# Optimization experiments

Hardware: AMD Instinct MI355X
Metric: run time of the kernel (lower is better)

Reference implementation:

```python
import jax, jax.numpy as jnp
import numpy as np
from jax.scipy.special import logsumexp

SPARSITY = 0.0


def setup_inputs() -> dict:
    key = jax.random.key(0)
    k1, k2, k3, k4, k5 = jax.random.split(key, 5)
    N, M = 65536, 1024
    sample = jax.random.uniform(k1, (N, 2), dtype=jnp.float32)
    mu = jax.random.uniform(k2, (M, 2), dtype=jnp.float32)
    sigma_log = jax.random.uniform(k3, (M, 2), dtype=jnp.float32)
    theta = jax.random.normal(k4, (M,), dtype=jnp.float32)
    w = jax.random.normal(k5, (M, 1), dtype=jnp.float32)
    return {"sample": sample, "mu": mu, "sigma_log": sigma_log, "theta": theta, "w": w}


def reference(sample, mu, sigma_log, theta, w):
    # Anisotropic covariance entries: gamma_j = R(theta)^T diag(sig2) R(theta)
    sig2 = jnp.exp(-2.0 * sigma_log)            # [M,2], inverse variances
    a, b = sig2[:, 0], sig2[:, 1]
    c, s = jnp.cos(theta), jnp.sin(theta)
    g11 = a * c**2 + b * s**2                   # [M]
    g12 = (a - b) * c * s                       # [M]
    g22 = a * s**2 + b * c**2                   # [M]

    # Log weights: log_softmax(w) - sum(sigma_log) (normalization factor)
    wlog = jax.nn.log_softmax(w, axis=0)[:, 0] - sigma_log.sum(axis=1)  # [M]

    # All-pairs anisotropic quadratic form, fused per-coordinate (no [N,M,2] tensor)
    dx = sample[:, None, 0] - mu[None, :, 0]    # [N,M]
    dy = sample[:, None, 1] - mu[None, :, 1]    # [N,M]
    qf = g11 * dx * dx + 2.0 * g12 * dx * dy + g22 * dy * dy  # [N,M]

    # Log-density at each sample: logsumexp over mixture components
    ll = logsumexp(wlog[None, :] - qf, axis=1)  # [N]

    # Negative log-likelihood + sparsity penalty
    nll = -ll.sum() + SPARSITY * jnp.sqrt(jax.nn.softmax(w, axis=0)).sum()
    return nll
```

## Files before the change

### kernel.cpp

```cpp
#include <hip/hip_runtime.h>
#include <math.h>

#define LOG2E 1.4426950408889634f
#define LN2   0.6931471805599453f

typedef float v2f __attribute__((ext_vector_type(2)));

__global__ __launch_bounds__(1024) void gm_params(
    const float* __restrict__ mu,
    const float* __restrict__ sigma_log,
    const float* __restrict__ theta,
    const float* __restrict__ w,
    float* __restrict__ pp,
    float* __restrict__ out)
{
    const int j = threadIdx.x;
    const int lane = j & 63;
    const int wid  = j >> 6;

    const float wj = w[j];

    float e = __expf(wj);
    #pragma unroll
    for (int off = 32; off > 0; off >>= 1)
        e += __shfl_down(e, off, 64);

    __shared__ float ws[16];
    if (lane == 0) ws[wid] = e;
    __syncthreads();

    float tot = 0.0f;
    #pragma unroll
    for (int k = 0; k < 16; ++k) tot += ws[k];
    const float lse = __logf(tot);

    const float sl0 = sigma_log[2 * j + 0];
    const float sl1 = sigma_log[2 * j + 1];
    const float a = __expf(-2.0f * sl0);
    const float b = __expf(-2.0f * sl1);
    const float th = theta[j];
    const float c = __cosf(th);
    const float s = __sinf(th);

    const float g11 = a * c * c + b * s * s;
    const float g12 = (a - b) * c * s;
    const float g22 = a * s * s + b * c * c;

    const float mx = mu[2 * j + 0];
    const float my = mu[2 * j + 1];

    const float wlog = wj - lse - (sl0 + sl1);

    const float A = g11;
    const float B = 2.0f * g12;
    const float C = g22;
    const float D = -(2.0f * g11 * mx + 2.0f * g12 * my);
    const float E = -(2.0f * g12 * mx + 2.0f * g22 * my);
    const float F = g11 * mx * mx + 2.0f * g12 * mx * my + g22 * my * my;
    const float K = (wlog - F) * LOG2E;

    const int base = 12 * (j >> 1) + (j & 1);
    pp[base + 0]  = -A * LOG2E;
    pp[base + 2]  = -B * LOG2E;
    pp[base + 4]  = -C * LOG2E;
    pp[base + 6]  = -D * LOG2E;
    pp[base + 8]  = -E * LOG2E;
    pp[base + 10] = K;

    if (j == 0) out[0] = 0.0f;
}

__global__ __launch_bounds__(1024) void gm_main(
    const float* __restrict__ sample,
    const float* __restrict__ pp,
    float* __restrict__ out,
    int M)
{
    const int lane = threadIdx.x & 63;
    int chunk = __builtin_amdgcn_readfirstlane((int)(threadIdx.x >> 6));
    chunk &= 15;
    __builtin_assume(chunk >= 0 && chunk < 16);

    const int i = blockIdx.x * 64 + lane;

    const float2 sv = ((const float2*)sample)[i];
    const float sx = sv.x, sy = sv.y;
    const v2f xx2 = (v2f)(sx * sx);
    const v2f xy2 = (v2f)(sx * sy);
    const v2f yy2 = (v2f)(sy * sy);
    const v2f sx2 = (v2f)(sx);
    const v2f sy2 = (v2f)(sy);

    const int pairs = M >> 5;
    const v2f* __restrict__ rec = (const v2f*)(pp + 12 * (chunk * pairs));

    v2f acc[4];
    #pragma unroll
    for (int u = 0; u < 4; ++u) acc[u] = (v2f)(0.0f);

    for (int p = 0; p < pairs; p += 4) {
        #pragma unroll
        for (int u = 0; u < 4; ++u) {
            const v2f* r = rec + 6 * (p + u);
            v2f e = r[5];
            e = __builtin_elementwise_fma(r[0], xx2, e);
            e = __builtin_elementwise_fma(r[1], xy2, e);
            e = __builtin_elementwise_fma(r[2], yy2, e);
            e = __builtin_elementwise_fma(r[3], sx2, e);
            e = __builtin_elementwise_fma(r[4], sy2, e);
            v2f ex;
            ex.x = __builtin_amdgcn_exp2f(e.x);
            ex.y = __builtin_amdgcn_exp2f(e.y);
            acc[u] += ex;
        }
    }

    const v2f accv = (acc[0] + acc[1]) + (acc[2] + acc[3]);

    __shared__ float psum[16][64];
    psum[chunk][lane] = accv.x + accv.y;
    __syncthreads();

    if (threadIdx.x < 64) {
        const int s = threadIdx.x;
        float tot = 0.0f;
        #pragma unroll
        for (int k = 0; k < 16; ++k) tot += psum[k][s];
        float v = -LN2 * __builtin_amdgcn_logf(tot);
        #pragma unroll
        for (int off = 32; off > 0; off >>= 1)
            v += __shfl_down(v, off, 64);
        if (s == 0) atomicAdd(out, v);
    }
}

extern "C" void kernel_launch(void* const* d_in, const int* in_sizes, int n_in,
                              void* d_out, int out_size, void* d_ws, size_t ws_size,
                              hipStream_t stream) {
    const float* sample    = (const float*)d_in[0];
    const float* mu        = (const float*)d_in[1];
    const float* sigma_log = (const float*)d_in[2];
    const float* theta     = (const float*)d_in[3];
    const float* w         = (const float*)d_in[4];
    float* out = (float*)d_out;
    float* pp = (float*)d_ws;

    const int M = in_sizes[3];
    const int N = in_sizes[0] / 2;

    gm_params<<<1, M, 0, stream>>>(mu, sigma_log, theta, w, pp, out);

    const int grid = N / 64;
    gm_main<<<grid, 1024, 0, stream>>>(sample, pp, out, M);
}
```

Measured before the change: 81.58 us.

## Fuse parameter precompute into main kernel with per-block LDS records

Removes the separate single-block parameter kernel. Each of the 1024 main blocks now recomputes all M component coefficients (softmax, exp, sin/cos) and stores them in shared memory, then reads them as float4 from LDS instead of from global memory. The output is zeroed with a memset instead. This drops one kernel launch and the serial dependency between the two kernels, at the cost of redundant per-block transcendental work plus an extra block-wide sync.

```diff
diff --git a/kernel.cpp b/kernel.cpp
--- a/kernel.cpp
+++ b/kernel.cpp
@@ -6,84 +6,75 @@
 
 typedef float v2f __attribute__((ext_vector_type(2)));
 
-__global__ __launch_bounds__(1024) void gm_params(
+__global__ __launch_bounds__(1024) void gm_fused(
+    const float* __restrict__ sample,
     const float* __restrict__ mu,
     const float* __restrict__ sigma_log,
     const float* __restrict__ theta,
     const float* __restrict__ w,
-    float* __restrict__ pp,
-    float* __restrict__ out)
+    float* __restrict__ out,
+    int M)
 {
-    const int j = threadIdx.x;
-    const int lane = j & 63;
-    const int wid  = j >> 6;
+    __shared__ float4 recs4[512 * 3];
+    __shared__ float  ws[16];
+    __shared__ float  psum[16][64];
 
-    const float wj = w[j];
+    const int tid  = threadIdx.x;
+    const int lane = tid & 63;
+    const int wid  = tid >> 6;
 
+    const int i = blockIdx.x * 64 + lane;
+    const float2 sv = ((const float2*)sample)[i];
+
+    const float wj = w[tid];
     float e = __expf(wj);
     #pragma unroll
     for (int off = 32; off > 0; off >>= 1)
         e += __shfl_down(e, off, 64);
-
-    __shared__ float ws[16];
     if (lane == 0) ws[wid] = e;
     __syncthreads();
-
     float tot = 0.0f;
     #pragma unroll
     for (int k = 0; k < 16; ++k) tot += ws[k];
     const float lse = __logf(tot);
 
-    const float sl0 = sigma_log[2 * j + 0];
-    const float sl1 = sigma_log[2 * j + 1];
-    const float a = __expf(-2.0f * sl0);
-    const float b = __expf(-2.0f * sl1);
-    const float th = theta[j];
-    const float c = __cosf(th);
-    const float s = __sinf(th);
+    {
+        const float sl0 = sigma_log[2 * tid + 0];
+        const float sl1 = sigma_log[2 * tid + 1];
+        const float a = __expf(-2.0f * sl0);
+        const float b = __expf(-2.0f * sl1);
+        const float th = theta[tid];
+        const float c = __cosf(th);
+        const float s = __sinf(th);
 
-    const float g11 = a * c * c + b * s * s;
-    const float g12 = (a - b) * c * s;
-    const float g22 = a * s * s + b * c * c;
+        const float g11 = a * c * c + b * s * s;
+        const float g12 = (a - b) * c * s;
+        const float g22 = a * s * s + b * c * c;
 
-    const float mx = mu[2 * j + 0];
-    const float my = mu[2 * j + 1];
+        const float mx = mu[2 * tid + 0];
+        const float my = mu[2 * tid + 1];
 
-    const float wlog = wj - lse - (sl0 + sl1);
+        const float wlog = wj - lse - (sl0 + sl1);
 
-    const float A = g11;
-    const float B = 2.0f * g12;
-    const float C = g22;
-    const float D = -(2.0f * g11 * mx + 2.0f * g12 * my);
-    const float E = -(2.0f * g12 * mx + 2.0f * g22 * my);
-    const float F = g11 * mx * mx + 2.0f * g12 * mx * my + g22 * my * my;
-    const float K = (wlog - F) * LOG2E;
+        const float A = g11;
+        const float B = 2.0f * g12;
+        const float C = g22;
+        const float D = -(2.0f * g11 * mx + 2.0f * g12 * my);
+        const float E = -(2.0f * g12 * mx + 2.0f * g22 * my);
+        const float F = g11 * mx * mx + 2.0f * g12 * mx * my + g22 * my * my;
+        const float K = (wlog - F) * LOG2E;
 
-    const int base = 12 * (j >> 1) + (j & 1);
-    pp[base + 0]  = -A * LOG2E;
-    pp[base + 2]  = -B * LOG2E;
-    pp[base + 4]  = -C * LOG2E;
-    pp[base + 6]  = -D * LOG2E;
-    pp[base + 8]  = -E * LOG2E;
-    pp[base + 10] = K;
+        float* recs = (float*)recs4;
+        const int base = 12 * (tid >> 1) + (tid & 1);
+        recs[base + 0]  = -A * LOG2E;
+        recs[base + 2]  = -B * LOG2E;
+        recs[base + 4]  = -C * LOG2E;
+        recs[base + 6]  = -D * LOG2E;
+        recs[base + 8]  = -E * LOG2E;
+        recs[base + 10] = K;
+    }
+    __syncthreads();
 
-    if (j == 0) out[0] = 0.0f;
-}
-
-__global__ __launch_bounds__(1024) void gm_main(
-    const float* __restrict__ sample,
-    const float* __restrict__ pp,
-    float* __restrict__ out,
-    int M)
-{
-    const int lane = threadIdx.x & 63;
-    int chunk = __builtin_amdgcn_readfirstlane((int)(threadIdx.x >> 6));
-    chunk &= 15;
-    __builtin_assume(chunk >= 0 && chunk < 16);
-
-    const int i = blockIdx.x * 64 + lane;
-
-    const float2 sv = ((const float2*)sample)[i];
     const float sx = sv.x, sy = sv.y;
     const v2f xx2 = (v2f)(sx * sx);
     const v2f xy2 = (v2f)(sx * sy);
@@ -92,7 +83,7 @@
     const v2f sy2 = (v2f)(sy);
 
     const int pairs = M >> 5;
-    const v2f* __restrict__ rec = (const v2f*)(pp + 12 * (chunk * pairs));
+    const int p0 = wid * pairs;
 
     v2f acc[4];
     #pragma unroll
@@ -101,36 +92,44 @@
     for (int p = 0; p < pairs; p += 4) {
         #pragma unroll
         for (int u = 0; u < 4; ++u) {
-            const v2f* r = rec + 6 * (p + u);
-            v2f e = r[5];
-            e = __builtin_elementwise_fma(r[0], xx2, e);
-            e = __builtin_elementwise_fma(r[1], xy2, e);
-            e = __builtin_elementwise_fma(r[2], yy2, e);
-            e = __builtin_elementwise_fma(r[3], sx2, e);
-            e = __builtin_elementwise_fma(r[4], sy2, e);
+            const float4* r4 = &recs4[3 * (p0 + p + u)];
+            const float4 r0 = r4[0];
+            const float4 r1 = r4[1];
+            const float4 r2 = r4[2];
+            const v2f ra = {r0.x, r0.y};
+            const v2f rb = {r0.z, r0.w};
+            const v2f rc = {r1.x, r1.y};
+            const v2f rd = {r1.z, r1.w};
+            const v2f re = {r2.x, r2.y};
+            const v2f rk = {r2.z, r2.w};
+
+            v2f ev = rk;
+            ev = __builtin_elementwise_fma(ra, xx2, ev);
+            ev = __builtin_elementwise_fma(rb, xy2, ev);
+            ev = __builtin_elementwise_fma(rc, yy2, ev);
+            ev = __builtin_elementwise_fma(rd, sx2, ev);
+            ev = __builtin_elementwise_fma(re, sy2, ev);
+
             v2f ex;
-            ex.x = __builtin_amdgcn_exp2f(e.x);
-            ex.y = __builtin_amdgcn_exp2f(e.y);
+            ex.x = __builtin_amdgcn_exp2f(ev.x);
+            ex.y = __builtin_amdgcn_exp2f(ev.y);
             acc[u] += ex;
         }
     }
 
     const v2f accv = (acc[0] + acc[1]) + (acc[2] + acc[3]);
-
-    __shared__ float psum[16][64];
-    psum[chunk][lane] = accv.x + accv.y;
+    psum[wid][lane] = accv.x + accv.y;
     __syncthreads();
 
-    if (threadIdx.x < 64) {
-        const int s = threadIdx.x;
-        float tot = 0.0f;
+    if (tid < 64) {
+        float t = 0.0f;
         #pragma unroll
-        for (int k = 0; k < 16; ++k) tot += psum[k][s];
-        float v = -LN2 * __builtin_amdgcn_logf(tot);
+        for (int k = 0; k < 16; ++k) t += psum[k][tid];
+        float v = -LN2 * __builtin_amdgcn_logf(t);
         #pragma unroll
         for (int off = 32; off > 0; off >>= 1)
             v += __shfl_down(v, off, 64);
-        if (s == 0) atomicAdd(out, v);
+        if (tid == 0) atomicAdd(out, v);
     }
 }
 
@@ -143,13 +142,12 @@
     const float* theta     = (const float*)d_in[3];
     const float* w         = (const float*)d_in[4];
     float* out = (float*)d_out;
-    float* pp = (float*)d_ws;
 
     const int M = in_sizes[3];
     const int N = in_sizes[0] / 2;
 
-    gm_params<<<1, M, 0, stream>>>(mu, sigma_log, theta, w, pp, out);
+    hipMemsetAsync(out, 0, sizeof(float), stream);
 
     const int grid = N / 64;
-    gm_main<<<grid, 1024, 0, stream>>>(sample, pp, out, M);
+    gm_fused<<<grid, 1024, 0, stream>>>(sample, mu, sigma_log, theta, w, out, M);
 }
```

New measurement: 80.35 us. Within noise of the previous version (-1.5%).
